# Performance work log

Hardware: AMD Instinct MI355X
Metric: run time of the kernel (lower is better)

Reference implementation:

```python
import jax, jax.numpy as jnp
import numpy as np

B, S, D = 8, 2048, 64
NEG = -1e9


def setup_inputs() -> dict:
    key = jax.random.key(0)
    kq, kk, kv = jax.random.split(key, 3)
    return {
        "queries": jax.random.normal(kq, (B, S, D), dtype=jnp.float32),
        "keys": jax.random.normal(kk, (B, S, D), dtype=jnp.float32),
        "values": jax.random.normal(kv, (B, S, D), dtype=jnp.float32),
        "mask_q": jnp.ones((B, S), dtype=jnp.float32),
        "mask_k": jnp.ones((B, S), dtype=jnp.float32),
        "mask_v": jnp.ones((B, S), dtype=jnp.float32),
    }


def reference(queries, keys, values, mask_q, mask_k, mask_v):
    # scaled QK^T: [B, Sq, Sk]
    scaler = jnp.sqrt(jnp.asarray(queries.shape[-1], dtype=queries.dtype))
    scores = jnp.einsum("bqd,bkd->bqk", queries, keys) / scaler
    # additive padding mask from outer product of query/key masks
    padding_mask = mask_q[:, :, None] * mask_k[:, None, :]  # [B, Sq, Sk]
    scores = scores + (1.0 - padding_mask) * NEG
    attention_weights = jax.nn.softmax(scores, axis=-1)
    # mask values then weighted sum
    values = values * mask_v[:, :, None]
    output = jnp.einsum("bqk,bkd->bqd", attention_weights, values)
    return output
```

## Files before the change

kernel.cpp:

```cpp
#include <hip/hip_runtime.h>
#include <hip/hip_bf16.h>
#include <math.h>

#define BATCH 8
#define SEQ   2048
#define DIM   64
#define NEGC  (-1e9f)
#define SPLIT 4
#define TPB   8

typedef short short8  __attribute__((ext_vector_type(8)));
typedef float f32x4   __attribute__((ext_vector_type(4)));
typedef float f32x16  __attribute__((ext_vector_type(16)));

#define MFMA32(a, b, c) __builtin_amdgcn_mfma_f32_32x32x16_bf16((a), (b), (c), 0, 0, 0)

__device__ __forceinline__ ushort f2bf(float x) {
    uint u = __float_as_uint(x);
    uint r = (u + 0x7fffu + ((u >> 16) & 1u)) >> 16;
    return (ushort)r;
}
__device__ __forceinline__ float bf2f(ushort h) {
    return __uint_as_float(((uint)h) << 16);
}

__global__ __launch_bounds__(256)
void prep_kv(const float* __restrict__ K, const float* __restrict__ V,
             const float* __restrict__ MV, ushort* __restrict__ ws) {
    __shared__ float raw[64 * 68];
    const int t    = threadIdx.x;
    const int isV  = blockIdx.x >> 8;
    const int img  = blockIdx.x & 255;
    const int b    = img >> 5;
    const int tile = img & 31;
    ushort* wsI = ws + (size_t)(b * 32 + tile) * 8192;

    if (!isV) {
        const float* Kb = K + ((size_t)b * SEQ + tile * 64) * DIM;
#pragma unroll
        for (int u = 0; u < 4; u++) {
            int f = t + 256 * u, key = f >> 4, d4 = (f & 15) * 4;
            *(float4*)&raw[key * 68 + d4] = *(const float4*)(Kb + (size_t)f * 4);
        }
        __syncthreads();
#pragma unroll
        for (int u = 0; u < 2; u++) {
            int r = t + 256 * u;
            int mt = r >> 8, kc = (r >> 6) & 3, L = r & 63;
            int key = mt * 32 + (L & 31), d0 = kc * 16 + (L >> 5) * 8;
            float4 x0 = *(float4*)&raw[key * 68 + d0];
            float4 x1 = *(float4*)&raw[key * 68 + d0 + 4];
            float xs[8] = {x0.x, x0.y, x0.z, x0.w, x1.x, x1.y, x1.z, x1.w};
            short8 hv;
#pragma unroll
            for (int j = 0; j < 8; j++) hv[j] = (short)f2bf(xs[j]);
            *(short8*)(wsI + r * 8) = hv;
        }
    } else {
        const float* Vb  = V  + ((size_t)b * SEQ + tile * 64) * DIM;
        const float* MVb = MV + (size_t)b * SEQ + tile * 64;
#pragma unroll
        for (int u = 0; u < 4; u++) {
            int f = t + 256 * u, key = f >> 4, d4 = (f & 15) * 4;
            float4 x = *(const float4*)(Vb + (size_t)f * 4);
            float mv = MVb[key];
            x.x *= mv; x.y *= mv; x.z *= mv; x.w *= mv;
            *(float4*)&raw[key * 68 + d4] = x;
        }
        __syncthreads();
#pragma unroll
        for (int u = 0; u < 2; u++) {
            int r = t + 256 * u;
            int dt = r >> 8, kc = (r >> 6) & 3, L = r & 63;
            int d = dt * 32 + (L & 31), k0 = kc * 16 + (L >> 5) * 8;
            short8 ov;
#pragma unroll
            for (int j = 0; j < 8; j++) ov[j] = (short)f2bf(raw[(k0 + j) * 68 + d]);
            *(short8*)(wsI + 4096 + r * 8) = ov;
        }
    }
}

__global__ __launch_bounds__(256, 4)
void attn_main(const float* __restrict__ Q, const float* __restrict__ MQ,
               const float* __restrict__ MK, const ushort* __restrict__ ws,
               float* __restrict__ PO, float* __restrict__ ML) {
    __shared__ __align__(16) ushort Stage[2][8192];

    const int t    = threadIdx.x;
    const int w    = t >> 6;
    const int lane = t & 63;
    const int h    = lane >> 5;
    const int lm   = lane & 31;
    const int qg   = w & 1;
    const int kh   = w >> 1;

    const int b  = blockIdx.x & 7;
    const int r  = blockIdx.x >> 3;
    const int s  = r & 3;
    const int qt = r >> 2;
    const int q  = qt * 64 + qg * 32 + lm;

    const float*  MKb  = MK + (size_t)b * SEQ;
    const ushort* wsKV = ws + (size_t)b * 32 * 8192;

    short8 qh[4], ql[4];
    {
        const float* Qr = Q + ((size_t)b * SEQ + q) * DIM;
#pragma unroll
        for (int kc = 0; kc < 4; kc++) {
            const float* p = Qr + kc * 16 + h * 8;
            float4 x0 = *(const float4*)p;
            float4 x1 = *(const float4*)(p + 4);
            float xs[8] = {x0.x, x0.y, x0.z, x0.w, x1.x, x1.y, x1.z, x1.w};
#pragma unroll
            for (int j = 0; j < 8; j++) {
                float v   = xs[j] * 0.125f;
                ushort hi = f2bf(v);
                ql[kc][j] = (short)f2bf(v - bf2f(hi));
                qh[kc][j] = (short)hi;
            }
        }
    }
    const float mq   = MQ[(size_t)b * SEQ + q];
    const float apen = NEGC * mq;

    float m = -1e30f, l = 0.0f;
    f32x16 ot0, ot1;
#pragma unroll
    for (int i = 0; i < 16; i++) { ot0[i] = 0.0f; ot1[i] = 0.0f; }

    {
        const ushort* src = wsKV + (size_t)(s * TPB) * 8192;
#pragma unroll
        for (int u = 0; u < 4; u++) {
            const int off = (u * 256 + w * 64 + lane) * 8;
            __builtin_amdgcn_global_load_lds(
                (const __attribute__((address_space(1))) void*)(src + off),
                (__attribute__((address_space(3))) void*)(&Stage[0][0] + off),
                16, 0, 0);
        }
    }
    __syncthreads();

    f32x4 mk[4];
#pragma unroll
    for (int v = 0; v < 4; v++)
        mk[v] = *(const f32x4*)(MKb + (s * TPB) * 64 + kh * 32 + v * 8 + h * 4);

#pragma unroll 1
    for (int tt = 0; tt < TPB; tt++) {
        const ushort* cur = &Stage[tt & 1][0];

        if (tt + 1 < TPB) {
            const ushort* src = wsKV + (size_t)(s * TPB + tt + 1) * 8192;
            ushort* dst = &Stage[(tt + 1) & 1][0];
#pragma unroll
            for (int u = 0; u < 4; u++) {
                const int off = (u * 256 + w * 64 + lane) * 8;
                __builtin_amdgcn_global_load_lds(
                    (const __attribute__((address_space(1))) void*)(src + off),
                    (__attribute__((address_space(3))) void*)(dst + off),
                    16, 0, 0);
            }
        }
        f32x4 nmk[4];
#pragma unroll
        for (int v = 0; v < 4; v++) nmk[v] = mk[v];
        if (tt + 1 < TPB) {
            const float* mkp = MKb + (s * TPB + tt + 1) * 64 + kh * 32 + h * 4;
#pragma unroll
            for (int v = 0; v < 4; v++) nmk[v] = *(const f32x4*)(mkp + v * 8);
        }

        f32x16 st;
#pragma unroll
        for (int i = 0; i < 16; i++) st[i] = 0.0f;
#pragma unroll
        for (int kc = 0; kc < 4; kc++) {
            short8 a = *(const short8*)&cur[((kh * 4 + kc) * 64 + lane) * 8];
            st = MFMA32(a, qh[kc], st);
            st = MFMA32(a, ql[kc], st);
        }

        float sv[16];
#pragma unroll
        for (int v = 0; v < 4; v++)
#pragma unroll
            for (int c = 0; c < 4; c++)
                sv[v * 4 + c] = st[v * 4 + c] + (NEGC - apen * mk[v][c]);
        float cm = sv[0];
#pragma unroll
        for (int i = 1; i < 16; i++) cm = fmaxf(cm, sv[i]);
        cm = fmaxf(cm, __shfl_xor(cm, 32));
        float nm    = fmaxf(m, cm);
        float alpha = __expf(m - nm);
        m = nm;

        float p[16], cs = 0.0f;
#pragma unroll
        for (int i = 0; i < 16; i++) { p[i] = __expf(sv[i] - nm); cs += p[i]; }
        cs += __shfl_xor(cs, 32);
        l   = l * alpha + cs;
        ot0 *= alpha; ot1 *= alpha;

        uint g[4][2], x[4][2];
#pragma unroll
        for (int v = 0; v < 4; v++) {
            __hip_bfloat162 c0 = __float22bfloat162_rn(make_float2(p[v*4+0], p[v*4+1]));
            __hip_bfloat162 c1 = __float22bfloat162_rn(make_float2(p[v*4+2], p[v*4+3]));
            __builtin_memcpy(&g[v][0], &c0, 4);
            __builtin_memcpy(&g[v][1], &c1, 4);
            x[v][0] = (uint)__shfl_xor((int)g[v][0], 32);
            x[v][1] = (uint)__shfl_xor((int)g[v][1], 32);
        }
        uint pbw[2][4];
        pbw[0][0] = h ? x[1][0] : g[0][0];
        pbw[0][1] = h ? x[1][1] : g[0][1];
        pbw[0][2] = h ? g[1][0] : x[0][0];
        pbw[0][3] = h ? g[1][1] : x[0][1];
        pbw[1][0] = h ? x[3][0] : g[2][0];
        pbw[1][1] = h ? x[3][1] : g[2][1];
        pbw[1][2] = h ? g[3][0] : x[2][0];
        pbw[1][3] = h ? g[3][1] : x[2][1];

#pragma unroll
        for (int c = 0; c < 2; c++) {
            short8 pb;
            __builtin_memcpy(&pb, &pbw[c][0], 16);
            short8 v0 = *(const short8*)&cur[4096 + ((0 * 4 + kh * 2 + c) * 64 + lane) * 8];
            short8 v1 = *(const short8*)&cur[4096 + ((1 * 4 + kh * 2 + c) * 64 + lane) * 8];
            ot0 = MFMA32(v0, pb, ot0);
            ot1 = MFMA32(v1, pb, ot1);
        }

#pragma unroll
        for (int v = 0; v < 4; v++) mk[v] = nmk[v];
        __syncthreads();
    }

    float* MscF = (float*)&Stage[0][0];
    if (kh == 1) {
        float* sc = MscF + (qg * 64 + lane) * 36;
#pragma unroll
        for (int i = 0; i < 16; i++) { sc[i] = ot0[i]; sc[16 + i] = ot1[i]; }
        sc[32] = m;
        sc[33] = l;
    }
    __syncthreads();
    if (kh == 0) {
        const float* sc = MscF + (qg * 64 + lane) * 36;
        float mb = sc[32], lb = sc[33];
        float nm = fmaxf(m, mb);
        float fa = __expf(m - nm);
        float fb = __expf(mb - nm);
        float lt = l * fa + lb * fb;

        float* po = PO + (((size_t)(s * 8 + b) * SEQ) + qt * 64 + qg * 32 + lm) * 64;
#pragma unroll
        for (int dt = 0; dt < 2; dt++) {
            const f32x16& o = dt ? ot1 : ot0;
#pragma unroll
            for (int rq = 0; rq < 4; rq++) {
                f32x4 rv;
#pragma unroll
                for (int c = 0; c < 4; c++)
                    rv[c] = o[rq * 4 + c] * fa + sc[dt * 16 + rq * 4 + c] * fb;
                __builtin_nontemporal_store(rv, (f32x4*)(po + dt * 32 + rq * 8 + h * 4));
            }
        }
        if (h == 0) {
            float* mlp = ML + 2 * (((size_t)(s * 8 + b) * SEQ) + qt * 64 + qg * 32 + lm);
            __builtin_nontemporal_store(nm, mlp + 0);
            __builtin_nontemporal_store(lt, mlp + 1);
        }
    }
}

__global__ __launch_bounds__(256)
void merge_o(const float* __restrict__ PO, const float* __restrict__ ML,
             float* __restrict__ O) {
    const int tid = blockIdx.x * 256 + threadIdx.x;
    const int qln = tid >> 4;
    const int dq  = tid & 15;
    const int b   = qln >> 11;
    const int qr  = qln & 2047;

    float2 mls[SPLIT];
#pragma unroll
    for (int s = 0; s < SPLIT; s++) {
        const float* mlp = ML + 2 * ((size_t)(s * 8 + b) * SEQ + qr);
        mls[s] = make_float2(mlp[0], mlp[1]);
    }
    float mm = mls[0].x;
#pragma unroll
    for (int s = 1; s < SPLIT; s++) mm = fmaxf(mm, mls[s].x);
    float f[SPLIT], denom = 0.0f;
#pragma unroll
    for (int s = 0; s < SPLIT; s++) {
        f[s] = __expf(mls[s].x - mm);
        denom += mls[s].y * f[s];
    }
    float inv = 1.0f / denom;

    const size_t POS = (size_t)8 * SEQ * 64;
    const size_t o0  = ((size_t)b * SEQ + qr) * 64 + dq * 4;
    f32x4 acc = {0, 0, 0, 0};
#pragma unroll
    for (int s = 0; s < SPLIT; s++) {
        f32x4 v = __builtin_nontemporal_load((const f32x4*)(PO + s * POS + o0));
        acc += v * f[s];
    }
    *(f32x4*)(O + ((size_t)b * SEQ + qr) * DIM + dq * 4) = acc * inv;
}

extern "C" void kernel_launch(void* const* d_in, const int* in_sizes, int n_in,
                              void* d_out, int out_size, void* d_ws, size_t ws_size,
                              hipStream_t stream) {
    const float* Q  = (const float*)d_in[0];
    const float* K  = (const float*)d_in[1];
    const float* V  = (const float*)d_in[2];
    const float* MQ = (const float*)d_in[3];
    const float* MK = (const float*)d_in[4];
    const float* MV = (const float*)d_in[5];
    float* O = (float*)d_out;

    ushort* wsKV = (ushort*)d_ws;
    float*  PO   = (float*)((char*)d_ws + (4u << 20));
    float*  ML   = (float*)((char*)d_ws + (20u << 20));

    prep_kv  <<<dim3(512),  dim3(256), 0, stream>>>(K, V, MV, wsKV);
    attn_main<<<dim3(1024), dim3(256), 0, stream>>>(Q, MQ, MK, wsKV, PO, ML);
    merge_o  <<<dim3(1024), dim3(256), 0, stream>>>(PO, ML, O);
}
```

Measured before the change: 105.4 us.

## Fuse split-K merge into attention kernel via last-block atomic counter

Removes the separate merge_o launch. Each attention block now increments a per-query-tile counter after writing its partial output, and the last of the four split blocks combines the partials into O. The counters are zeroed in prep_kv. Block indexing is remapped so the splits of one query tile sit next to each other, and the partial stores become normal cached stores so the merging block can read them back from cache. The hi/lo bf16 QK MFMA chain is also split into two independent accumulators to shorten the dependency chain. The cost is added fences, an atomic per block, and a serialized merge tail in the last block of each tile.

```diff
diff --git a/kernel.cpp b/kernel.cpp
--- a/kernel.cpp
+++ b/kernel.cpp
@@ -26,7 +26,8 @@
 
 __global__ __launch_bounds__(256)
 void prep_kv(const float* __restrict__ K, const float* __restrict__ V,
-             const float* __restrict__ MV, ushort* __restrict__ ws) {
+             const float* __restrict__ MV, ushort* __restrict__ ws,
+             int* __restrict__ CNT) {
     __shared__ float raw[64 * 68];
     const int t    = threadIdx.x;
     const int isV  = blockIdx.x >> 8;
@@ -34,6 +35,8 @@
     const int b    = img >> 5;
     const int tile = img & 31;
     ushort* wsI = ws + (size_t)(b * 32 + tile) * 8192;
+
+    if (blockIdx.x == 0) CNT[t] = 0;
 
     if (!isV) {
         const float* Kb = K + ((size_t)b * SEQ + tile * 64) * DIM;
@@ -84,8 +87,10 @@
 __global__ __launch_bounds__(256, 4)
 void attn_main(const float* __restrict__ Q, const float* __restrict__ MQ,
                const float* __restrict__ MK, const ushort* __restrict__ ws,
-               float* __restrict__ PO, float* __restrict__ ML) {
+               float* __restrict__ PO, float* __restrict__ ML,
+               int* __restrict__ CNT, float* __restrict__ O) {
     __shared__ __align__(16) ushort Stage[2][8192];
+    __shared__ int winFlag;
 
     const int t    = threadIdx.x;
     const int w    = t >> 6;
@@ -95,10 +100,10 @@
     const int qg   = w & 1;
     const int kh   = w >> 1;
 
-    const int b  = blockIdx.x & 7;
-    const int r  = blockIdx.x >> 3;
-    const int s  = r & 3;
-    const int qt = r >> 2;
+    const int s  = blockIdx.x & 3;
+    const int qb = blockIdx.x >> 2;
+    const int b  = qb >> 5;
+    const int qt = qb & 31;
     const int q  = qt * 64 + qg * 32 + lm;
 
     const float*  MKb  = MK + (size_t)b * SEQ;
@@ -173,14 +178,14 @@
             for (int v = 0; v < 4; v++) nmk[v] = *(const f32x4*)(mkp + v * 8);
         }
 
-        f32x16 st;
-#pragma unroll
-        for (int i = 0; i < 16; i++) st[i] = 0.0f;
+        f32x16 stA, stB;
+#pragma unroll
+        for (int i = 0; i < 16; i++) { stA[i] = 0.0f; stB[i] = 0.0f; }
 #pragma unroll
         for (int kc = 0; kc < 4; kc++) {
             short8 a = *(const short8*)&cur[((kh * 4 + kc) * 64 + lane) * 8];
-            st = MFMA32(a, qh[kc], st);
-            st = MFMA32(a, ql[kc], st);
+            stA = MFMA32(a, qh[kc], stA);
+            stB = MFMA32(a, ql[kc], stB);
         }
 
         float sv[16];
@@ -188,7 +193,8 @@
         for (int v = 0; v < 4; v++)
 #pragma unroll
             for (int c = 0; c < 4; c++)
-                sv[v * 4 + c] = st[v * 4 + c] + (NEGC - apen * mk[v][c]);
+                sv[v * 4 + c] = (stA[v * 4 + c] + stB[v * 4 + c])
+                                + (NEGC - apen * mk[v][c]);
         float cm = sv[0];
 #pragma unroll
         for (int i = 1; i < 16; i++) cm = fmaxf(cm, sv[i]);
@@ -266,52 +272,59 @@
 #pragma unroll
                 for (int c = 0; c < 4; c++)
                     rv[c] = o[rq * 4 + c] * fa + sc[dt * 16 + rq * 4 + c] * fb;
-                __builtin_nontemporal_store(rv, (f32x4*)(po + dt * 32 + rq * 8 + h * 4));
+                *(f32x4*)(po + dt * 32 + rq * 8 + h * 4) = rv;
             }
         }
         if (h == 0) {
             float* mlp = ML + 2 * (((size_t)(s * 8 + b) * SEQ) + qt * 64 + qg * 32 + lm);
-            __builtin_nontemporal_store(nm, mlp + 0);
-            __builtin_nontemporal_store(lt, mlp + 1);
-        }
-    }
-}
-
-__global__ __launch_bounds__(256)
-void merge_o(const float* __restrict__ PO, const float* __restrict__ ML,
-             float* __restrict__ O) {
-    const int tid = blockIdx.x * 256 + threadIdx.x;
-    const int qln = tid >> 4;
-    const int dq  = tid & 15;
-    const int b   = qln >> 11;
-    const int qr  = qln & 2047;
-
-    float2 mls[SPLIT];
-#pragma unroll
-    for (int s = 0; s < SPLIT; s++) {
-        const float* mlp = ML + 2 * ((size_t)(s * 8 + b) * SEQ + qr);
-        mls[s] = make_float2(mlp[0], mlp[1]);
-    }
-    float mm = mls[0].x;
-#pragma unroll
-    for (int s = 1; s < SPLIT; s++) mm = fmaxf(mm, mls[s].x);
-    float f[SPLIT], denom = 0.0f;
-#pragma unroll
-    for (int s = 0; s < SPLIT; s++) {
-        f[s] = __expf(mls[s].x - mm);
-        denom += mls[s].y * f[s];
-    }
-    float inv = 1.0f / denom;
-
-    const size_t POS = (size_t)8 * SEQ * 64;
-    const size_t o0  = ((size_t)b * SEQ + qr) * 64 + dq * 4;
-    f32x4 acc = {0, 0, 0, 0};
-#pragma unroll
-    for (int s = 0; s < SPLIT; s++) {
-        f32x4 v = __builtin_nontemporal_load((const f32x4*)(PO + s * POS + o0));
-        acc += v * f[s];
-    }
-    *(f32x4*)(O + ((size_t)b * SEQ + qr) * DIM + dq * 4) = acc * inv;
+            mlp[0] = nm;
+            mlp[1] = lt;
+        }
+        __threadfence();
+    }
+    __syncthreads();
+    if (t == 0) {
+        int old = atomicAdd(&CNT[b * 32 + qt], 1);
+        winFlag = (old == 3);
+    }
+    __syncthreads();
+
+    if (winFlag) {
+        __threadfence();
+        const int qq = t >> 2;
+        const int dc = t & 3;
+        const size_t qrow = (size_t)qt * 64 + qq;
+
+        float2 a[SPLIT];
+#pragma unroll
+        for (int sp = 0; sp < SPLIT; sp++) {
+            const float* mlp = ML + 2 * ((size_t)(sp * 8 + b) * SEQ + qrow);
+            a[sp] = make_float2(mlp[0], mlp[1]);
+        }
+        float mm = a[0].x;
+#pragma unroll
+        for (int sp = 1; sp < SPLIT; sp++) mm = fmaxf(mm, a[sp].x);
+        float f[SPLIT], denom = 0.0f;
+#pragma unroll
+        for (int sp = 0; sp < SPLIT; sp++) {
+            f[sp] = __expf(a[sp].x - mm);
+            denom += a[sp].y * f[sp];
+        }
+        float inv = 1.0f / denom;
+
+        float* Orow = O + ((size_t)b * SEQ + qrow) * DIM + dc * 16;
+#pragma unroll
+        for (int i = 0; i < 4; i++) {
+            f32x4 acc = {0, 0, 0, 0};
+#pragma unroll
+            for (int sp = 0; sp < SPLIT; sp++) {
+                const float* po = PO + ((size_t)(sp * 8 + b) * SEQ + qrow) * 64
+                                     + dc * 16 + i * 4;
+                acc += (*(const f32x4*)po) * f[sp];
+            }
+            *(f32x4*)(Orow + i * 4) = acc * inv;
+        }
+    }
 }
 
 extern "C" void kernel_launch(void* const* d_in, const int* in_sizes, int n_in,
@@ -328,8 +341,8 @@
     ushort* wsKV = (ushort*)d_ws;
     float*  PO   = (float*)((char*)d_ws + (4u << 20));
     float*  ML   = (float*)((char*)d_ws + (20u << 20));
-
-    prep_kv  <<<dim3(512),  dim3(256), 0, stream>>>(K, V, MV, wsKV);
-    attn_main<<<dim3(1024), dim3(256), 0, stream>>>(Q, MQ, MK, wsKV, PO, ML);
-    merge_o  <<<dim3(1024), dim3(256), 0, stream>>>(PO, ML, O);
-}
+    int*    CNT  = (int*)((char*)d_ws + (21u << 20));
+
+    prep_kv  <<<dim3(512),  dim3(256), 0, stream>>>(K, V, MV, wsKV, CNT);
+    attn_main<<<dim3(1024), dim3(256), 0, stream>>>(Q, MQ, MK, wsKV, PO, ML, CNT, O);
+}
```

Measured after the change: 249.1 us. 2.36x slower.
